# Kernel tuning notes

Hardware: AMD Instinct MI355X
Metric: run time of the kernel (lower is better)

Reference implementation:

```python
import jax, jax.numpy as jnp
import numpy as np

NUM_HEADS = 16
KERNEL_SIZE = 13


def setup_inputs() -> dict:
    key = jax.random.key(0)
    ks = jax.random.split(key, 6)
    B, L, C = 4, 4096, 512
    H, K = NUM_HEADS, KERNEL_SIZE
    x = jax.random.normal(ks[0], (B, L, C), dtype=jnp.float32)
    qkv_w = jax.random.normal(ks[1], (C, 3 * C), dtype=jnp.float32) * 0.02
    qkv_b = jnp.zeros((3 * C,), dtype=jnp.float32)
    rpb = jax.random.normal(ks[2], (H, 2 * K - 1), dtype=jnp.float32) * 0.02
    proj_w = jax.random.normal(ks[3], (C, C), dtype=jnp.float32) * 0.02
    proj_b = jnp.zeros((C,), dtype=jnp.float32)
    return {"x": x, "qkv_w": qkv_w, "qkv_b": qkv_b, "rpb": rpb,
            "proj_w": proj_w, "proj_b": proj_b}


def reference(x, qkv_w, qkv_b, rpb, proj_w, proj_b):
    B, L, C = x.shape
    H, K = NUM_HEADS, KERNEL_SIZE
    hd = C // H
    scale = hd ** -0.5
    kh = K // 2

    # qkv projection -> q,k,v each [B,H,L,hd]
    qkv = (x @ qkv_w + qkv_b).reshape(B, L, 3, H, hd).transpose(2, 0, 3, 1, 4)
    q, k, v = qkv[0] * scale, qkv[1], qkv[2]

    # NATTEN window: start index clamped so window stays in-bounds
    pos = jnp.arange(L)
    ni = jnp.clip(pos - kh, 0, L - K)              # [L] window start per query
    idx = ni[:, None] + jnp.arange(K)[None, :]     # [L,K] key positions
    # rpb index: (key_pos - query_pos) + (K-1)
    rpb_idx = (ni - pos + (K - 1))[:, None] + jnp.arange(K)[None, :]  # [L,K]

    k_win = k[:, :, idx, :]                        # [B,H,L,K,hd]
    v_win = v[:, :, idx, :]                        # [B,H,L,K,hd]

    attn = jnp.einsum('bhld,bhlkd->bhlk', q, k_win) + rpb[:, rpb_idx][None]
    attn = jax.nn.softmax(attn, axis=-1)

    out = jnp.einsum('bhlk,bhlkd->bhld', attn, v_win)  # [B,H,L,hd]
    out = out.transpose(0, 2, 1, 3).reshape(B, L, C)
    return out @ proj_w + proj_b
```

## Files before the change

### kernel.cpp

```cpp
#include <hip/hip_runtime.h>
#include <hip/hip_bf16.h>
#include <stdint.h>


typedef __attribute__((ext_vector_type(8))) short short8;
typedef __attribute__((ext_vector_type(4))) float f32x4;
typedef __attribute__((ext_vector_type(8))) unsigned short u16x8;
typedef __attribute__((ext_vector_type(4))) float float4v;

#define NB 4
#define NL 4096
#define NC 512
#define NH 16
#define HD 32
#define KW 13
#define KHALF 6
#define NM (NB*NL)

__device__ __forceinline__ float b2f(unsigned short u) {
  union { unsigned int i; float f; } x; x.i = ((unsigned int)u) << 16; return x.f;
}
__device__ __forceinline__ unsigned short f2b(float f) {
  __hip_bfloat16 h = __float2bfloat16(f);
  return __builtin_bit_cast(unsigned short, h);
}
__device__ __forceinline__ void gll16(const unsigned short* g, unsigned short* l) {
  __builtin_amdgcn_global_load_lds(
      (const __attribute__((address_space(1))) void*)g,
      (__attribute__((address_space(3))) void*)l, 16, 0, 0);
}

__global__ __launch_bounds__(256) void cvt_f32_bf16(const float* __restrict__ in,
                                                    unsigned short* __restrict__ out) {
  long i = (long)blockIdx.x * 256 + threadIdx.x;
  const float4v* in4 = (const float4v*)in;
  float4v a = in4[i * 2];
  float4v b = in4[i * 2 + 1];
  u16x8 u;
  u[0] = f2b(a.x); u[1] = f2b(a.y); u[2] = f2b(a.z); u[3] = f2b(a.w);
  u[4] = f2b(b.x); u[5] = f2b(b.y); u[6] = f2b(b.z); u[7] = f2b(b.w);
  ((u16x8*)out)[i] = u;
}

__global__ __launch_bounds__(256)
void pack_bf(const float* __restrict__ W, unsigned short* __restrict__ Bf,
             int N, int ngroups) {
  int g = blockIdx.x * 256 + threadIdx.x;
  if (g >= ngroups) return;
  int lane = g & 63;
  int kb   = (g >> 6) & 1;
  int nj   = (g >> 7) & 3;
  int wn   = (g >> 9) & 1;
  int kt   = (g >> 10) & 7;
  int tn   = g >> 13;
  int n  = tn * 128 + wn * 64 + nj * 16 + (lane & 15);
  int k0 = kt * 64 + (kb * 4 + (lane >> 4)) * 8;
  u16x8 u;
  #pragma unroll
  for (int e = 0; e < 8; ++e) u[e] = f2b(W[(long)(k0 + e) * N + n]);
  ((u16x8*)Bf)[g] = u;
}


__device__ __forceinline__ void stage_tileA(const unsigned short* __restrict__ G,
                                            long rowBase, int K, int kt,
                                            unsigned short* ldsDst, int tid) {
  int r  = tid >> 3;
  int ch = (tid & 7) ^ (r & 7);
  const unsigned short* s0 = G + (rowBase + r) * (long)K + kt * 64 + ch * 8;
  unsigned short* d0 = ldsDst + tid * 8;
  #pragma unroll
  for (int q = 0; q < 4; ++q)
    gll16(s0 + (long)32 * q * K, d0 + 2048 * q);
}

#define BAR() __builtin_amdgcn_s_barrier()
#define LGK0() do { asm volatile("s_waitcnt lgkmcnt(0)" ::: "memory"); \
                    __builtin_amdgcn_sched_barrier(0); } while (0)
#define VM(N) asm volatile("s_waitcnt vmcnt(" #N ")" ::: "memory")

#define LDA(ABASE) do { \
  const char* _ba = (const char*)(ABASE); \
  _Pragma("unroll") for (int ii = 0; ii < 4; ++ii) { \
    int _row = wm*64 + ii*16 + lr; \
    _Pragma("unroll") for (int kb = 0; kb < 2; ++kb) \
      af[ii][kb] = *(const short8*)(_ba + _row*128 + (((kb*4+lk) ^ lr7) * 16)); \
  } \
} while (0)

#define LDBG(KT) do { \
  const short8* _bp = (const short8*)(Bfw + (long)(KT) * 8192) + lane; \
  _Pragma("unroll") for (int nj = 0; nj < 4; ++nj) \
    _Pragma("unroll") for (int kb = 0; kb < 2; ++kb) \
      bf[nj][kb] = _bp[(nj*2 + kb) * 64]; \
} while (0)

#define MMA_ALL() do { \
  __builtin_amdgcn_s_setprio(1); \
  _Pragma("unroll") for (int ii = 0; ii < 4; ++ii) \
    _Pragma("unroll") for (int jj = 0; jj < 4; ++jj) \
      _Pragma("unroll") for (int kb = 0; kb < 2; ++kb) \
        acc[ii][jj] = __builtin_amdgcn_mfma_f32_16x16x32_bf16( \
            af[ii][kb], bf[jj][kb], acc[ii][jj], 0, 0, 0); \
  __builtin_amdgcn_s_setprio(0); \
} while (0)

#define GTILE(ABUF, KT, STG, VMARG) do { \
  LDBG(KT); \
  LDA(ABUF); \
  LGK0(); \
  BAR(); \
  if (STG) stage_tileA(Ag, mBase, K, (KT) + 2, ABUF, tid); \
  VMARG; \
  MMA_ALL(); \
  BAR(); \
} while (0)

template<int OUT_BF16>
__global__ __launch_bounds__(256, 3)
void gemm128(const unsigned short* __restrict__ Ag,
             const unsigned short* __restrict__ Bf,
             const float* __restrict__ bias,
             void* __restrict__ Cout,
             int M, int N, int K, int tilesN) {
  __shared__ __align__(16) unsigned short lds[16384];

  int tid = threadIdx.x;
  int nwg = gridDim.x;
  int cpx = nwg >> 3;
  int wg  = ((int)blockIdx.x & 7) * cpx + ((int)blockIdx.x >> 3);
  int tm = wg / tilesN, tn = wg % tilesN;
  long mBase = (long)tm * 128;
  long nBase = (long)tn * 128;

  int lane = tid & 63, wave = tid >> 6;
  int wm = wave >> 1;
  int wn = wave & 1;
  int lr = lane & 15, lk = lane >> 4, lr7 = lr & 7;

  const unsigned short* Bfw = Bf + (long)tn * 65536 + wn * 4096;

  unsigned short* A0 = lds;
  unsigned short* A1 = lds + 8192;

  f32x4 acc[4][4];
  #pragma unroll
  for (int i = 0; i < 4; ++i)
    #pragma unroll
    for (int j = 0; j < 4; ++j) acc[i][j] = (f32x4){0.f, 0.f, 0.f, 0.f};

  short8 af[4][2], bf[4][2];

  stage_tileA(Ag, mBase, K, 0, A0, tid);
  stage_tileA(Ag, mBase, K, 1, A1, tid);
  VM(4);
  BAR();

  #pragma unroll 1
  for (int i = 0; i < 3; ++i) {
    GTILE(A0, 2*i,     true, VM(4));
    GTILE(A1, 2*i + 1, true, VM(4));
  }
  GTILE(A0, 6, false, VM(0));
  GTILE(A1, 7, false, VM(0));

  long rowb = mBase + wm * 64 + (lane >> 4) * 4;
  int  colb = (int)nBase + wn * 64 + lr;
  if (OUT_BF16) {
    unsigned short* C = (unsigned short*)Cout;
    #pragma unroll
    for (int mi = 0; mi < 4; ++mi)
      #pragma unroll
      for (int nj = 0; nj < 4; ++nj) {
        int col = colb + nj * 16;
        float bv = bias[col];
        #pragma unroll
        for (int r = 0; r < 4; ++r)
          C[(rowb + mi * 16 + r) * (long)N + col] = f2b(acc[mi][nj][r] + bv);
      }
  } else {
    float* C = (float*)Cout;
    #pragma unroll
    for (int mi = 0; mi < 4; ++mi)
      #pragma unroll
      for (int nj = 0; nj < 4; ++nj) {
        int col = colb + nj * 16;
        float bv = bias[col];
        #pragma unroll
        for (int r = 0; r < 4; ++r)
          C[(rowb + mi * 16 + r) * (long)N + col] = acc[mi][nj][r] + bv;
      }
  }
}

__global__ __launch_bounds__(256)
void natt(const unsigned short* __restrict__ qkv, const float* __restrict__ rpb,
          unsigned short* __restrict__ out) {
  int tid = blockIdx.x * 256 + threadIdx.x;
  int h = tid & 15;
  int l = (tid >> 4) & (NL - 1);
  int b = tid >> 16;
  const float scale = 0.17677669529663687f;

  long qb = ((long)(b * NL + l) * 3) * NC + h * HD;
  float q[HD];
  {
    const u16x8* q8 = (const u16x8*)(qkv + qb);
    #pragma unroll
    for (int w = 0; w < 4; ++w) {
      u16x8 u = q8[w];
      #pragma unroll
      for (int e = 0; e < 8; ++e) q[w * 8 + e] = b2f(u[e]) * scale;
    }
  }

  int ni = l - KHALF;
  if (ni < 0) ni = 0;
  if (ni > NL - KW) ni = NL - KW;
  const float* rb = rpb + h * (2 * KW - 1) + (ni - l + KW - 1);

  float p[KW];
  float mx = -1e30f;
  #pragma unroll
  for (int j = 0; j < KW; ++j) {
    long kb = ((long)(b * NL + ni + j) * 3 + 1) * NC + h * HD;
    const u16x8* k8 = (const u16x8*)(qkv + kb);
    float s = 0.f;
    #pragma unroll
    for (int w = 0; w < 4; ++w) {
      u16x8 u = k8[w];
      #pragma unroll
      for (int e = 0; e < 8; ++e) s += q[w * 8 + e] * b2f(u[e]);
    }
    s += rb[j];
    p[j] = s;
    mx = fmaxf(mx, s);
  }

  float sum = 0.f;
  #pragma unroll
  for (int j = 0; j < KW; ++j) { p[j] = __expf(p[j] - mx); sum += p[j]; }
  float inv = 1.0f / sum;

  float o[HD];
  #pragma unroll
  for (int d = 0; d < HD; ++d) o[d] = 0.f;
  #pragma unroll
  for (int j = 0; j < KW; ++j) {
    long vb = ((long)(b * NL + ni + j) * 3 + 2) * NC + h * HD;
    const u16x8* v8 = (const u16x8*)(qkv + vb);
    float wj = p[j] * inv;
    #pragma unroll
    for (int w = 0; w < 4; ++w) {
      u16x8 u = v8[w];
      #pragma unroll
      for (int e = 0; e < 8; ++e) o[w * 8 + e] += wj * b2f(u[e]);
    }
  }

  unsigned short* op = out + (long)(b * NL + l) * NC + h * HD;
  #pragma unroll
  for (int w = 0; w < 4; ++w) {
    u16x8 u;
    #pragma unroll
    for (int e = 0; e < 8; ++e) u[e] = f2b(o[w * 8 + e]);
    *((u16x8*)(op + w * 8)) = u;
  }
}

extern "C" void kernel_launch(void* const* d_in, const int* in_sizes, int n_in,
                              void* d_out, int out_size, void* d_ws, size_t ws_size,
                              hipStream_t stream) {
  const float* x      = (const float*)d_in[0];
  const float* qkv_w  = (const float*)d_in[1];
  const float* qkv_b  = (const float*)d_in[2];
  const float* rpb    = (const float*)d_in[3];
  const float* proj_w = (const float*)d_in[4];
  const float* proj_b = (const float*)d_in[5];
  float* out = (float*)d_out;

  char* ws = (char*)d_ws;
  unsigned short* xb   = (unsigned short*)(ws);
  unsigned short* Bf1  = (unsigned short*)(ws + 16777216);
  unsigned short* Bf2  = (unsigned short*)(ws + 18350080);
  unsigned short* qkvo = (unsigned short*)(ws + 18874368);
  unsigned short* attno= (unsigned short*)(ws + 69206016);

  cvt_f32_bf16<<<dim3(4096), dim3(256), 0, stream>>>(x, xb);
  pack_bf<<<dim3(384), dim3(256), 0, stream>>>(qkv_w, Bf1, 1536, 98304);
  pack_bf<<<dim3(128), dim3(256), 0, stream>>>(proj_w, Bf2, 512, 32768);
  gemm128<1><<<dim3(1536), dim3(256), 0, stream>>>(xb, Bf1, qkv_b, qkvo,
                                                   NM, 1536, 512, 12);
  natt<<<dim3(1024), dim3(256), 0, stream>>>(qkvo, rpb, attno);
  gemm128<0><<<dim3(512), dim3(256), 0, stream>>>(attno, Bf2, proj_b, out,
                                                  NM, 512, 512, 4);
}
```

Measured before the change: 97.41 us.

## Fuse fp32-to-bf16 input conversion into QKV GEMM A-tile loading

Removes the standalone conversion kernel and has the QKV GEMM load fp32 activations directly into registers, convert them to bf16 and write them into swizzled LDS. This eliminates one launch and the write and re-read of a bf16 copy of x. In exchange, each column-tile workgroup reads twice the bytes for A. The async global-to-LDS staging is replaced by register-staged loads with an extra barrier per k-tile, which may reduce overlap and increase register pressure.

```diff
diff --git a/kernel.cpp b/kernel.cpp
--- a/kernel.cpp
+++ b/kernel.cpp
@@ -28,18 +28,6 @@
   __builtin_amdgcn_global_load_lds(
       (const __attribute__((address_space(1))) void*)g,
       (__attribute__((address_space(3))) void*)l, 16, 0, 0);
-}
-
-__global__ __launch_bounds__(256) void cvt_f32_bf16(const float* __restrict__ in,
-                                                    unsigned short* __restrict__ out) {
-  long i = (long)blockIdx.x * 256 + threadIdx.x;
-  const float4v* in4 = (const float4v*)in;
-  float4v a = in4[i * 2];
-  float4v b = in4[i * 2 + 1];
-  u16x8 u;
-  u[0] = f2b(a.x); u[1] = f2b(a.y); u[2] = f2b(a.z); u[3] = f2b(a.w);
-  u[4] = f2b(b.x); u[5] = f2b(b.y); u[6] = f2b(b.z); u[7] = f2b(b.w);
-  ((u16x8*)out)[i] = u;
 }
 
 __global__ __launch_bounds__(256)
@@ -74,10 +62,39 @@
     gll16(s0 + (long)32 * q * K, d0 + 2048 * q);
 }
 
+__device__ __forceinline__ void loadA_f32(const float* __restrict__ G,
+                                          long rowBase, int K, int kt,
+                                          int tid, float4v (&ra)[8]) {
+  int r  = tid >> 3;
+  int ch = tid & 7;
+  const float* s = G + (rowBase + r) * (long)K + kt * 64 + ch * 8;
+  #pragma unroll
+  for (int q = 0; q < 4; ++q) {
+    const float4v* p = (const float4v*)(s + (long)32 * q * K);
+    ra[2 * q]     = p[0];
+    ra[2 * q + 1] = p[1];
+  }
+}
+__device__ __forceinline__ void writeA_bf16(unsigned short* ldsA, int tid,
+                                            const float4v (&ra)[8]) {
+  int r  = tid >> 3;
+  int ch = tid & 7;
+  #pragma unroll
+  for (int q = 0; q < 4; ++q) {
+    int row = r + 32 * q;
+    const float4v a = ra[2 * q], b = ra[2 * q + 1];
+    u16x8 u;
+    u[0] = f2b(a.x); u[1] = f2b(a.y); u[2] = f2b(a.z); u[3] = f2b(a.w);
+    u[4] = f2b(b.x); u[5] = f2b(b.y); u[6] = f2b(b.z); u[7] = f2b(b.w);
+    *(u16x8*)(ldsA + row * 64 + ((ch ^ (row & 7)) * 8)) = u;
+  }
+}
+
 #define BAR() __builtin_amdgcn_s_barrier()
 #define LGK0() do { asm volatile("s_waitcnt lgkmcnt(0)" ::: "memory"); \
                     __builtin_amdgcn_sched_barrier(0); } while (0)
 #define VM(N) asm volatile("s_waitcnt vmcnt(" #N ")" ::: "memory")
+#define SCHED0() __builtin_amdgcn_sched_barrier(0)
 
 #define LDA(ABASE) do { \
   const char* _ba = (const char*)(ABASE); \
@@ -105,20 +122,32 @@
   __builtin_amdgcn_s_setprio(0); \
 } while (0)
 
-#define GTILE(ABUF, KT, STG, VMARG) do { \
+#define GTILE_BF16(ABUF, KT, STG, VMARG) do { \
   LDBG(KT); \
   LDA(ABUF); \
   LGK0(); \
   BAR(); \
-  if (STG) stage_tileA(Ag, mBase, K, (KT) + 2, ABUF, tid); \
+  if (STG) stage_tileA(Agh, mBase, K, (KT) + 2, ABUF, tid); \
   VMARG; \
   MMA_ALL(); \
   BAR(); \
 } while (0)
 
-template<int OUT_BF16>
+#define GTILE_F32(ABUF, KT, STG) do { \
+  LDBG(KT); \
+  SCHED0();  \
+  if (STG) loadA_f32(Agf, mBase, K, (KT) + 2, tid, ra); \
+  LDA(ABUF); \
+  LGK0(); \
+  MMA_ALL(); \
+  BAR(); \
+  if (STG) { writeA_bf16(ABUF, tid, ra); LGK0(); } \
+  BAR(); \
+} while (0)
+
+template<int OUT_BF16, int IN_F32>
 __global__ __launch_bounds__(256, 3)
-void gemm128(const unsigned short* __restrict__ Ag,
+void gemm128(const void* __restrict__ Ag,
              const unsigned short* __restrict__ Bf,
              const float* __restrict__ bias,
              void* __restrict__ Cout,
@@ -139,30 +168,54 @@
   int lr = lane & 15, lk = lane >> 4, lr7 = lr & 7;
 
   const unsigned short* Bfw = Bf + (long)tn * 65536 + wn * 4096;
+  const unsigned short* Agh = (const unsigned short*)Ag;
+  const float*          Agf = (const float*)Ag;
 
   unsigned short* A0 = lds;
   unsigned short* A1 = lds + 8192;
 
+  short8 af[4][2], bf[4][2];
   f32x4 acc[4][4];
-  #pragma unroll
-  for (int i = 0; i < 4; ++i)
-    #pragma unroll
-    for (int j = 0; j < 4; ++j) acc[i][j] = (f32x4){0.f, 0.f, 0.f, 0.f};
-
-  short8 af[4][2], bf[4][2];
-
-  stage_tileA(Ag, mBase, K, 0, A0, tid);
-  stage_tileA(Ag, mBase, K, 1, A1, tid);
-  VM(4);
-  BAR();
-
-  #pragma unroll 1
-  for (int i = 0; i < 3; ++i) {
-    GTILE(A0, 2*i,     true, VM(4));
-    GTILE(A1, 2*i + 1, true, VM(4));
-  }
-  GTILE(A0, 6, false, VM(0));
-  GTILE(A1, 7, false, VM(0));
+
+  if constexpr (IN_F32) {
+    float4v ra[8];
+    loadA_f32(Agf, mBase, K, 0, tid, ra);
+    writeA_bf16(A0, tid, ra);
+    loadA_f32(Agf, mBase, K, 1, tid, ra);
+    writeA_bf16(A1, tid, ra);
+    LGK0(); BAR();
+
+    #pragma unroll
+    for (int i = 0; i < 4; ++i)
+      #pragma unroll
+      for (int j = 0; j < 4; ++j) acc[i][j] = (f32x4){0.f, 0.f, 0.f, 0.f};
+
+    #pragma unroll 1
+    for (int i = 0; i < 3; ++i) {
+      GTILE_F32(A0, 2*i,     true);
+      GTILE_F32(A1, 2*i + 1, true);
+    }
+    GTILE_F32(A0, 6, false);
+    GTILE_F32(A1, 7, false);
+  } else {
+    stage_tileA(Agh, mBase, K, 0, A0, tid);
+    stage_tileA(Agh, mBase, K, 1, A1, tid);
+    VM(4);
+    BAR();
+
+    #pragma unroll
+    for (int i = 0; i < 4; ++i)
+      #pragma unroll
+      for (int j = 0; j < 4; ++j) acc[i][j] = (f32x4){0.f, 0.f, 0.f, 0.f};
+
+    #pragma unroll 1
+    for (int i = 0; i < 3; ++i) {
+      GTILE_BF16(A0, 2*i,     true, VM(4));
+      GTILE_BF16(A1, 2*i + 1, true, VM(4));
+    }
+    GTILE_BF16(A0, 6, false, VM(0));
+    GTILE_BF16(A1, 7, false, VM(0));
+  }
 
   long rowb = mBase + wm * 64 + (lane >> 4) * 4;
   int  colb = (int)nBase + wn * 64 + lr;
@@ -280,18 +333,16 @@
   float* out = (float*)d_out;
 
   char* ws = (char*)d_ws;
-  unsigned short* xb   = (unsigned short*)(ws);
-  unsigned short* Bf1  = (unsigned short*)(ws + 16777216);
-  unsigned short* Bf2  = (unsigned short*)(ws + 18350080);
-  unsigned short* qkvo = (unsigned short*)(ws + 18874368);
-  unsigned short* attno= (unsigned short*)(ws + 69206016);
-
-  cvt_f32_bf16<<<dim3(4096), dim3(256), 0, stream>>>(x, xb);
+  unsigned short* Bf1  = (unsigned short*)(ws);
+  unsigned short* Bf2  = (unsigned short*)(ws + 1572864);
+  unsigned short* qkvo = (unsigned short*)(ws + 2097152);
+  unsigned short* attno= (unsigned short*)(ws + 52428800);
+
   pack_bf<<<dim3(384), dim3(256), 0, stream>>>(qkv_w, Bf1, 1536, 98304);
   pack_bf<<<dim3(128), dim3(256), 0, stream>>>(proj_w, Bf2, 512, 32768);
-  gemm128<1><<<dim3(1536), dim3(256), 0, stream>>>(xb, Bf1, qkv_b, qkvo,
-                                                   NM, 1536, 512, 12);
+  gemm128<1, 1><<<dim3(1536), dim3(256), 0, stream>>>(x, Bf1, qkv_b, qkvo,
+                                                      NM, 1536, 512, 12);
   natt<<<dim3(1024), dim3(256), 0, stream>>>(qkvo, rpb, attno);
-  gemm128<0><<<dim3(512), dim3(256), 0, stream>>>(attno, Bf2, proj_b, out,
-                                                  NM, 512, 512, 4);
-}
+  gemm128<0, 0><<<dim3(512), dim3(256), 0, stream>>>(attno, Bf2, proj_b, out,
+                                                     NM, 512, 512, 4);
+}
```

New measurement: 117.3 us. 20.4% more time.

## Fuse f32-to-bf16 input conversion into QKV GEMM A-tile staging

Applied to the files above, without the earlier changes.

Removes the standalone conversion kernel for x and has the QKV GEMM stream f32 A tiles directly into LDS via global_load_lds, converting to bf16 when reading fragments for MFMA. This drops a full read/write pass and a launch. In exchange, A-tile global traffic and LDS footprint double, occupancy bound drops from 3 to 2 blocks per CU, and conversion is repeated for each N tile.

```diff
diff --git a/kernel.cpp b/kernel.cpp
--- a/kernel.cpp
+++ b/kernel.cpp
@@ -24,22 +24,16 @@
   __hip_bfloat16 h = __float2bfloat16(f);
   return __builtin_bit_cast(unsigned short, h);
 }
-__device__ __forceinline__ void gll16(const unsigned short* g, unsigned short* l) {
+__device__ __forceinline__ void gll16(const void* g, unsigned short* l) {
   __builtin_amdgcn_global_load_lds(
       (const __attribute__((address_space(1))) void*)g,
       (__attribute__((address_space(3))) void*)l, 16, 0, 0);
 }
-
-__global__ __launch_bounds__(256) void cvt_f32_bf16(const float* __restrict__ in,
-                                                    unsigned short* __restrict__ out) {
-  long i = (long)blockIdx.x * 256 + threadIdx.x;
-  const float4v* in4 = (const float4v*)in;
-  float4v a = in4[i * 2];
-  float4v b = in4[i * 2 + 1];
+__device__ __forceinline__ short8 pack8(float4v lo, float4v hi) {
   u16x8 u;
-  u[0] = f2b(a.x); u[1] = f2b(a.y); u[2] = f2b(a.z); u[3] = f2b(a.w);
-  u[4] = f2b(b.x); u[5] = f2b(b.y); u[6] = f2b(b.z); u[7] = f2b(b.w);
-  ((u16x8*)out)[i] = u;
+  u[0] = f2b(lo.x); u[1] = f2b(lo.y); u[2] = f2b(lo.z); u[3] = f2b(lo.w);
+  u[4] = f2b(hi.x); u[5] = f2b(hi.y); u[6] = f2b(hi.z); u[7] = f2b(hi.w);
+  return __builtin_bit_cast(short8, u);
 }
 
 __global__ __launch_bounds__(256)
@@ -61,32 +55,10 @@
   ((u16x8*)Bf)[g] = u;
 }
 
-
-__device__ __forceinline__ void stage_tileA(const unsigned short* __restrict__ G,
-                                            long rowBase, int K, int kt,
-                                            unsigned short* ldsDst, int tid) {
-  int r  = tid >> 3;
-  int ch = (tid & 7) ^ (r & 7);
-  const unsigned short* s0 = G + (rowBase + r) * (long)K + kt * 64 + ch * 8;
-  unsigned short* d0 = ldsDst + tid * 8;
-  #pragma unroll
-  for (int q = 0; q < 4; ++q)
-    gll16(s0 + (long)32 * q * K, d0 + 2048 * q);
-}
-
 #define BAR() __builtin_amdgcn_s_barrier()
 #define LGK0() do { asm volatile("s_waitcnt lgkmcnt(0)" ::: "memory"); \
                     __builtin_amdgcn_sched_barrier(0); } while (0)
 #define VM(N) asm volatile("s_waitcnt vmcnt(" #N ")" ::: "memory")
-
-#define LDA(ABASE) do { \
-  const char* _ba = (const char*)(ABASE); \
-  _Pragma("unroll") for (int ii = 0; ii < 4; ++ii) { \
-    int _row = wm*64 + ii*16 + lr; \
-    _Pragma("unroll") for (int kb = 0; kb < 2; ++kb) \
-      af[ii][kb] = *(const short8*)(_ba + _row*128 + (((kb*4+lk) ^ lr7) * 16)); \
-  } \
-} while (0)
 
 #define LDBG(KT) do { \
   const short8* _bp = (const short8*)(Bfw + (long)(KT) * 8192) + lane; \
@@ -105,25 +77,54 @@
   __builtin_amdgcn_s_setprio(0); \
 } while (0)
 
-#define GTILE(ABUF, KT, STG, VMARG) do { \
+
+__device__ __forceinline__ void stageA_f32(const float* __restrict__ G,
+                                           long rowBase, int K, int kt,
+                                           unsigned short* ldsDst, int tid) {
+  int lane = tid & 63, w = tid >> 6;
+  int rsub = lane >> 4;
+  int slot = lane & 15;
+  #pragma unroll
+  for (int q = 0; q < 8; ++q) {
+    int row = w * 32 + q * 4 + rsub;
+    int g = slot ^ (row & 15);
+    const float* src = G + (rowBase + row) * (long)K + kt * 64 + g * 4;
+    gll16(src, ldsDst + row * 128 + slot * 8);
+  }
+}
+
+#define LDA_F32(ABASE) do { \
+  const char* _ba = (const char*)(ABASE); \
+  _Pragma("unroll") for (int ii = 0; ii < 4; ++ii) { \
+    int _row = wm*64 + ii*16 + lr; \
+    const char* _rp = _ba + _row*256; \
+    _Pragma("unroll") for (int kb = 0; kb < 2; ++kb) { \
+      int _g = (kb*4 + lk) * 2; \
+      float4v _lo = *(const float4v*)(_rp + ((_g ^ lr) * 16)); \
+      float4v _hi = *(const float4v*)(_rp + (((_g+1) ^ lr) * 16)); \
+      af[ii][kb] = pack8(_lo, _hi); \
+    } \
+  } \
+} while (0)
+
+#define G1TILE(ABUF, KT, STG, VMARG) do { \
   LDBG(KT); \
-  LDA(ABUF); \
+  LDA_F32(ABUF); \
   LGK0(); \
   BAR(); \
-  if (STG) stage_tileA(Ag, mBase, K, (KT) + 2, ABUF, tid); \
+  if (STG) stageA_f32(Ag, mBase, K, (KT) + 2, ABUF, tid); \
   VMARG; \
   MMA_ALL(); \
   BAR(); \
 } while (0)
 
-template<int OUT_BF16>
-__global__ __launch_bounds__(256, 3)
-void gemm128(const unsigned short* __restrict__ Ag,
-             const unsigned short* __restrict__ Bf,
-             const float* __restrict__ bias,
-             void* __restrict__ Cout,
-             int M, int N, int K, int tilesN) {
-  __shared__ __align__(16) unsigned short lds[16384];
+__global__ __launch_bounds__(256, 2)
+void gemm128f(const float* __restrict__ Ag,
+              const unsigned short* __restrict__ Bf,
+              const float* __restrict__ bias,
+              unsigned short* __restrict__ Cout,
+              int M, int N, int K, int tilesN) {
+  __shared__ __align__(16) unsigned short lds[32768];
 
   int tid = threadIdx.x;
   int nwg = gridDim.x;
@@ -134,8 +135,99 @@
   long nBase = (long)tn * 128;
 
   int lane = tid & 63, wave = tid >> 6;
-  int wm = wave >> 1;
-  int wn = wave & 1;
+  int wm = wave >> 1, wn = wave & 1;
+  int lr = lane & 15, lk = lane >> 4;
+
+  const unsigned short* Bfw = Bf + (long)tn * 65536 + wn * 4096;
+
+  unsigned short* A0 = lds;
+  unsigned short* A1 = lds + 16384;
+
+  f32x4 acc[4][4];
+  #pragma unroll
+  for (int i = 0; i < 4; ++i)
+    #pragma unroll
+    for (int j = 0; j < 4; ++j) acc[i][j] = (f32x4){0.f, 0.f, 0.f, 0.f};
+
+  short8 af[4][2], bf[4][2];
+
+  stageA_f32(Ag, mBase, K, 0, A0, tid);
+  stageA_f32(Ag, mBase, K, 1, A1, tid);
+  VM(8);
+  BAR();
+
+  #pragma unroll 1
+  for (int i = 0; i < 3; ++i) {
+    G1TILE(A0, 2*i,     true, VM(8));
+    G1TILE(A1, 2*i + 1, true, VM(8));
+  }
+  G1TILE(A0, 6, false, VM(0));
+  G1TILE(A1, 7, false, VM(0));
+
+  long rowb = mBase + wm * 64 + (lane >> 4) * 4;
+  int  colb = (int)nBase + wn * 64 + lr;
+  #pragma unroll
+  for (int mi = 0; mi < 4; ++mi)
+    #pragma unroll
+    for (int nj = 0; nj < 4; ++nj) {
+      int col = colb + nj * 16;
+      float bv = bias[col];
+      #pragma unroll
+      for (int r = 0; r < 4; ++r)
+        Cout[(rowb + mi * 16 + r) * (long)N + col] = f2b(acc[mi][nj][r] + bv);
+    }
+}
+
+__device__ __forceinline__ void stage_tileA(const unsigned short* __restrict__ G,
+                                            long rowBase, int K, int kt,
+                                            unsigned short* ldsDst, int tid) {
+  int r  = tid >> 3;
+  int ch = (tid & 7) ^ (r & 7);
+  const unsigned short* s0 = G + (rowBase + r) * (long)K + kt * 64 + ch * 8;
+  unsigned short* d0 = ldsDst + tid * 8;
+  #pragma unroll
+  for (int q = 0; q < 4; ++q)
+    gll16(s0 + (long)32 * q * K, d0 + 2048 * q);
+}
+
+#define LDA_B16(ABASE) do { \
+  const char* _ba = (const char*)(ABASE); \
+  _Pragma("unroll") for (int ii = 0; ii < 4; ++ii) { \
+    int _row = wm*64 + ii*16 + lr; \
+    _Pragma("unroll") for (int kb = 0; kb < 2; ++kb) \
+      af[ii][kb] = *(const short8*)(_ba + _row*128 + (((kb*4+lk) ^ lr7) * 16)); \
+  } \
+} while (0)
+
+#define G2TILE(ABUF, KT, STG, VMARG) do { \
+  LDBG(KT); \
+  LDA_B16(ABUF); \
+  LGK0(); \
+  BAR(); \
+  if (STG) stage_tileA(Ag, mBase, K, (KT) + 2, ABUF, tid); \
+  VMARG; \
+  MMA_ALL(); \
+  BAR(); \
+} while (0)
+
+__global__ __launch_bounds__(256, 3)
+void gemm128b(const unsigned short* __restrict__ Ag,
+              const unsigned short* __restrict__ Bf,
+              const float* __restrict__ bias,
+              float* __restrict__ Cout,
+              int M, int N, int K, int tilesN) {
+  __shared__ __align__(16) unsigned short lds[16384];
+
+  int tid = threadIdx.x;
+  int nwg = gridDim.x;
+  int cpx = nwg >> 3;
+  int wg  = ((int)blockIdx.x & 7) * cpx + ((int)blockIdx.x >> 3);
+  int tm = wg / tilesN, tn = wg % tilesN;
+  long mBase = (long)tm * 128;
+  long nBase = (long)tn * 128;
+
+  int lane = tid & 63, wave = tid >> 6;
+  int wm = wave >> 1, wn = wave & 1;
   int lr = lane & 15, lk = lane >> 4, lr7 = lr & 7;
 
   const unsigned short* Bfw = Bf + (long)tn * 65536 + wn * 4096;
@@ -158,39 +250,24 @@
 
   #pragma unroll 1
   for (int i = 0; i < 3; ++i) {
-    GTILE(A0, 2*i,     true, VM(4));
-    GTILE(A1, 2*i + 1, true, VM(4));
-  }
-  GTILE(A0, 6, false, VM(0));
-  GTILE(A1, 7, false, VM(0));
+    G2TILE(A0, 2*i,     true, VM(4));
+    G2TILE(A1, 2*i + 1, true, VM(4));
+  }
+  G2TILE(A0, 6, false, VM(0));
+  G2TILE(A1, 7, false, VM(0));
 
   long rowb = mBase + wm * 64 + (lane >> 4) * 4;
   int  colb = (int)nBase + wn * 64 + lr;
-  if (OUT_BF16) {
-    unsigned short* C = (unsigned short*)Cout;
-    #pragma unroll
-    for (int mi = 0; mi < 4; ++mi)
-      #pragma unroll
-      for (int nj = 0; nj < 4; ++nj) {
-        int col = colb + nj * 16;
-        float bv = bias[col];
-        #pragma unroll
-        for (int r = 0; r < 4; ++r)
-          C[(rowb + mi * 16 + r) * (long)N + col] = f2b(acc[mi][nj][r] + bv);
-      }
-  } else {
-    float* C = (float*)Cout;
-    #pragma unroll
-    for (int mi = 0; mi < 4; ++mi)
-      #pragma unroll
-      for (int nj = 0; nj < 4; ++nj) {
-        int col = colb + nj * 16;
-        float bv = bias[col];
-        #pragma unroll
-        for (int r = 0; r < 4; ++r)
-          C[(rowb + mi * 16 + r) * (long)N + col] = acc[mi][nj][r] + bv;
-      }
-  }
+  #pragma unroll
+  for (int mi = 0; mi < 4; ++mi)
+    #pragma unroll
+    for (int nj = 0; nj < 4; ++nj) {
+      int col = colb + nj * 16;
+      float bv = bias[col];
+      #pragma unroll
+      for (int r = 0; r < 4; ++r)
+        Cout[(rowb + mi * 16 + r) * (long)N + col] = acc[mi][nj][r] + bv;
+    }
 }
 
 __global__ __launch_bounds__(256)
@@ -280,18 +357,16 @@
   float* out = (float*)d_out;
 
   char* ws = (char*)d_ws;
-  unsigned short* xb   = (unsigned short*)(ws);
-  unsigned short* Bf1  = (unsigned short*)(ws + 16777216);
-  unsigned short* Bf2  = (unsigned short*)(ws + 18350080);
-  unsigned short* qkvo = (unsigned short*)(ws + 18874368);
-  unsigned short* attno= (unsigned short*)(ws + 69206016);
-
-  cvt_f32_bf16<<<dim3(4096), dim3(256), 0, stream>>>(x, xb);
+  unsigned short* Bf1  = (unsigned short*)(ws);
+  unsigned short* Bf2  = (unsigned short*)(ws + 1572864);
+  unsigned short* qkvo = (unsigned short*)(ws + 2097152);
+  unsigned short* attno= (unsigned short*)(ws + 52428800);
+
   pack_bf<<<dim3(384), dim3(256), 0, stream>>>(qkv_w, Bf1, 1536, 98304);
   pack_bf<<<dim3(128), dim3(256), 0, stream>>>(proj_w, Bf2, 512, 32768);
-  gemm128<1><<<dim3(1536), dim3(256), 0, stream>>>(xb, Bf1, qkv_b, qkvo,
-                                                   NM, 1536, 512, 12);
+  gemm128f<<<dim3(1536), dim3(256), 0, stream>>>(x, Bf1, qkv_b, qkvo,
+                                                 NM, 1536, 512, 12);
   natt<<<dim3(1024), dim3(256), 0, stream>>>(qkvo, rpb, attno);
-  gemm128<0><<<dim3(512), dim3(256), 0, stream>>>(attno, Bf2, proj_b, out,
-                                                  NM, 512, 512, 4);
-}
+  gemm128b<<<dim3(512), dim3(256), 0, stream>>>(attno, Bf2, proj_b, out,
+                                                NM, 512, 512, 4);
+}
```

Result: slower. 103.4 us (+6.2%).

## Double-buffer B fragments in GEMM, drop trailing barrier, merge weight-pack launches

Applied to the files above, without the earlier changes.

The GEMM main loop now prefetches the next k-tile's B fragments from global memory into a second register set while the current tile's MFMAs run. The K loop is fully unrolled with explicit vmcnt waits, and the per-tile trailing barrier is removed. The two weight-packing kernels are merged into one launch to save launch overhead. In exchange, register pressure rises from the second B buffer, which may hurt occupancy at 3 blocks per SM. The hand-tuned wait counts also have to match the actual load ordering.

```diff
diff --git a/kernel.cpp b/kernel.cpp
--- a/kernel.cpp
+++ b/kernel.cpp
@@ -24,7 +24,7 @@
   __hip_bfloat16 h = __float2bfloat16(f);
   return __builtin_bit_cast(unsigned short, h);
 }
-__device__ __forceinline__ void gll16(const unsigned short* g, unsigned short* l) {
+__device__ __forceinline__ void gll16(const void* g, unsigned short* l) {
   __builtin_amdgcn_global_load_lds(
       (const __attribute__((address_space(1))) void*)g,
       (__attribute__((address_space(3))) void*)l, 16, 0, 0);
@@ -42,11 +42,9 @@
   ((u16x8*)out)[i] = u;
 }
 
-__global__ __launch_bounds__(256)
-void pack_bf(const float* __restrict__ W, unsigned short* __restrict__ Bf,
-             int N, int ngroups) {
-  int g = blockIdx.x * 256 + threadIdx.x;
-  if (g >= ngroups) return;
+__device__ __forceinline__ void pack_one(const float* __restrict__ W,
+                                         unsigned short* __restrict__ Bf,
+                                         int N, int g) {
   int lane = g & 63;
   int kb   = (g >> 6) & 1;
   int nj   = (g >> 7) & 3;
@@ -60,6 +58,18 @@
   for (int e = 0; e < 8; ++e) u[e] = f2b(W[(long)(k0 + e) * N + n]);
   ((u16x8*)Bf)[g] = u;
 }
+__global__ __launch_bounds__(256)
+void pack_both(const float* __restrict__ W1, unsigned short* __restrict__ Bf1,
+               const float* __restrict__ W2, unsigned short* __restrict__ Bf2) {
+  int g = blockIdx.x * 256 + threadIdx.x;
+  if (g < 98304) pack_one(W1, Bf1, 1536, g);
+  else           pack_one(W2, Bf2, 512, g - 98304);
+}
+
+#define BAR() __builtin_amdgcn_s_barrier()
+#define LGK0() do { asm volatile("s_waitcnt lgkmcnt(0)" ::: "memory"); \
+                    __builtin_amdgcn_sched_barrier(0); } while (0)
+#define VM(N) asm volatile("s_waitcnt vmcnt(" #N ")" ::: "memory")
 
 
 __device__ __forceinline__ void stage_tileA(const unsigned short* __restrict__ G,
@@ -74,12 +84,7 @@
     gll16(s0 + (long)32 * q * K, d0 + 2048 * q);
 }
 
-#define BAR() __builtin_amdgcn_s_barrier()
-#define LGK0() do { asm volatile("s_waitcnt lgkmcnt(0)" ::: "memory"); \
-                    __builtin_amdgcn_sched_barrier(0); } while (0)
-#define VM(N) asm volatile("s_waitcnt vmcnt(" #N ")" ::: "memory")
-
-#define LDA(ABASE) do { \
+#define LDA_B16(ABASE) do { \
   const char* _ba = (const char*)(ABASE); \
   _Pragma("unroll") for (int ii = 0; ii < 4; ++ii) { \
     int _row = wm*64 + ii*16 + lr; \
@@ -88,32 +93,31 @@
   } \
 } while (0)
 
-#define LDBG(KT) do { \
+#define LDBG_TO(BF, KT) do { \
   const short8* _bp = (const short8*)(Bfw + (long)(KT) * 8192) + lane; \
   _Pragma("unroll") for (int nj = 0; nj < 4; ++nj) \
     _Pragma("unroll") for (int kb = 0; kb < 2; ++kb) \
-      bf[nj][kb] = _bp[(nj*2 + kb) * 64]; \
+      BF[nj][kb] = _bp[(nj*2 + kb) * 64]; \
 } while (0)
 
-#define MMA_ALL() do { \
+#define MMA_ALL(BF) do { \
   __builtin_amdgcn_s_setprio(1); \
   _Pragma("unroll") for (int ii = 0; ii < 4; ++ii) \
     _Pragma("unroll") for (int jj = 0; jj < 4; ++jj) \
       _Pragma("unroll") for (int kb = 0; kb < 2; ++kb) \
         acc[ii][jj] = __builtin_amdgcn_mfma_f32_16x16x32_bf16( \
-            af[ii][kb], bf[jj][kb], acc[ii][jj], 0, 0, 0); \
+            af[ii][kb], BF[jj][kb], acc[ii][jj], 0, 0, 0); \
   __builtin_amdgcn_s_setprio(0); \
 } while (0)
 
-#define GTILE(ABUF, KT, STG, VMARG) do { \
-  LDBG(KT); \
-  LDA(ABUF); \
+#define GT(ABUF, KT, BFC, BFN, DO_LDBG, STG, VMARG) do { \
+  if (DO_LDBG) LDBG_TO(BFN, (KT) + 1); \
+  LDA_B16(ABUF); \
   LGK0(); \
+  VMARG; \
   BAR(); \
   if (STG) stage_tileA(Ag, mBase, K, (KT) + 2, ABUF, tid); \
-  VMARG; \
-  MMA_ALL(); \
-  BAR(); \
+  MMA_ALL(BFC); \
 } while (0)
 
 template<int OUT_BF16>
@@ -134,8 +138,7 @@
   long nBase = (long)tn * 128;
 
   int lane = tid & 63, wave = tid >> 6;
-  int wm = wave >> 1;
-  int wn = wave & 1;
+  int wm = wave >> 1, wn = wave & 1;
   int lr = lane & 15, lk = lane >> 4, lr7 = lr & 7;
 
   const unsigned short* Bfw = Bf + (long)tn * 65536 + wn * 4096;
@@ -149,20 +152,22 @@
     #pragma unroll
     for (int j = 0; j < 4; ++j) acc[i][j] = (f32x4){0.f, 0.f, 0.f, 0.f};
 
-  short8 af[4][2], bf[4][2];
+  short8 af[4][2], bfA[4][2], bfB[4][2];
 
   stage_tileA(Ag, mBase, K, 0, A0, tid);
   stage_tileA(Ag, mBase, K, 1, A1, tid);
-  VM(4);
+  LDBG_TO(bfA, 0);
+  VM(12);
   BAR();
 
-  #pragma unroll 1
-  for (int i = 0; i < 3; ++i) {
-    GTILE(A0, 2*i,     true, VM(4));
-    GTILE(A1, 2*i + 1, true, VM(4));
-  }
-  GTILE(A0, 6, false, VM(0));
-  GTILE(A1, 7, false, VM(0));
+  GT(A0, 0, bfA, bfB, 1, 1, VM(16));
+  GT(A1, 1, bfB, bfA, 1, 1, VM(8));
+  GT(A0, 2, bfA, bfB, 1, 1, VM(8));
+  GT(A1, 3, bfB, bfA, 1, 1, VM(8));
+  GT(A0, 4, bfA, bfB, 1, 1, VM(8));
+  GT(A1, 5, bfB, bfA, 1, 1, VM(8));
+  GT(A0, 6, bfA, bfB, 1, 0, VM(8));
+  GT(A1, 7, bfB, bfA, 0, 0, (void)0);
 
   long rowb = mBase + wm * 64 + (lane >> 4) * 4;
   int  colb = (int)nBase + wn * 64 + lr;
@@ -287,8 +292,7 @@
   unsigned short* attno= (unsigned short*)(ws + 69206016);
 
   cvt_f32_bf16<<<dim3(4096), dim3(256), 0, stream>>>(x, xb);
-  pack_bf<<<dim3(384), dim3(256), 0, stream>>>(qkv_w, Bf1, 1536, 98304);
-  pack_bf<<<dim3(128), dim3(256), 0, stream>>>(proj_w, Bf2, 512, 32768);
+  pack_both<<<dim3(512), dim3(256), 0, stream>>>(qkv_w, Bf1, proj_w, Bf2);
   gemm128<1><<<dim3(1536), dim3(256), 0, stream>>>(xb, Bf1, qkv_b, qkvo,
                                                    NM, 1536, 512, 12);
   natt<<<dim3(1024), dim3(256), 0, stream>>>(qkvo, rpb, attno);
```

After: 115.3 us. 1.18x slower.
